# Performance work log

Hardware: AMD Instinct MI355X
Metric: run time of the kernel (lower is better)

Reference implementation:

```python
import jax, jax.numpy as jnp
import numpy as np


def setup_inputs() -> dict:
    key = jax.random.key(0)
    k1, k2 = jax.random.split(key)
    B, H, W, D = 2, 160, 192, 160
    X = jax.random.normal(k1, (B, H, W, D, 2), dtype=jnp.float32)
    deformation = jax.random.normal(k2, (B, H, W, D, 3), dtype=jnp.float32)
    return {"X": X, "deformation": deformation}


def reference(X, deformation):
    # X: (B,H,W,D,2); warp the first channel by the dense deformation field.
    B, H, W, D, _ = X.shape
    Y = X[..., 0:1]                     # (B,H,W,D,1) volume to warp
    N = H * W * D

    # Identity grid, matching tf.meshgrid(x,y,z) 'xy' semantics: shape (H,W,D),
    # x varies along axis1 (width), y along axis0 (height), z along axis2 (depth).
    ys, xs, zs = jnp.meshgrid(
        jnp.arange(H, dtype=jnp.float32),
        jnp.arange(W, dtype=jnp.float32),
        jnp.arange(D, dtype=jnp.float32),
        indexing='ij')

    d = deformation.reshape(B, N, 3)
    x = xs.reshape(-1)[None, :] + d[..., 0]   # (B,N)
    y = ys.reshape(-1)[None, :] + d[..., 1]
    z = zs.reshape(-1)[None, :] + d[..., 2]

    x0 = jnp.floor(x).astype(jnp.int32); x1 = x0 + 1
    y0 = jnp.floor(y).astype(jnp.int32); y1 = y0 + 1
    z0 = jnp.floor(z).astype(jnp.int32); z1 = z0 + 1

    x0 = jnp.clip(x0, 0, W - 1); x1 = jnp.clip(x1, 0, W - 1)
    y0 = jnp.clip(y0, 0, H - 1); y1 = jnp.clip(y1, 0, H - 1)
    z0 = jnp.clip(z0, 0, D - 1); z1 = jnp.clip(z1, 0, D - 1)

    flat = Y.reshape(B, N, 1)           # (B, H*W*D, C=1)

    def gather(yy, xx, zz):
        idx = (yy * (W * D) + xx * D + zz)[..., None]   # (B,N,1)
        return jnp.take_along_axis(flat, idx, axis=1)

    p000 = gather(y0, x0, z0); p001 = gather(y0, x0, z1)
    p010 = gather(y0, x1, z0); p011 = gather(y0, x1, z1)
    p100 = gather(y1, x0, z0); p101 = gather(y1, x0, z1)
    p110 = gather(y1, x1, z0); p111 = gather(y1, x1, z1)

    # Weights use the CLIPPED corner coordinates (faithful to the original).
    x0f = x0.astype(jnp.float32); x1f = x1.astype(jnp.float32)
    y0f = y0.astype(jnp.float32); y1f = y1.astype(jnp.float32)
    z0f = z0.astype(jnp.float32); z1f = z1.astype(jnp.float32)

    w000 = ((y1f - y) * (x1f - x) * (z1f - z))[..., None]
    w001 = ((y1f - y) * (x1f - x) * (z - z0f))[..., None]
    w010 = ((y1f - y) * (x - x0f) * (z1f - z))[..., None]
    w011 = ((y1f - y) * (x - x0f) * (z - z0f))[..., None]
    w100 = ((y - y0f) * (x1f - x) * (z1f - z))[..., None]
    w101 = ((y - y0f) * (x1f - x) * (z - z0f))[..., None]
    w110 = ((y - y0f) * (x - x0f) * (z1f - z))[..., None]
    w111 = ((y - y0f) * (x - x0f) * (z - z0f))[..., None]

    out = (w000 * p000 + w001 * p001 + w010 * p010 + w011 * p011 +
           w100 * p100 + w101 * p101 + w110 * p110 + w111 * p111)
    return out.reshape(B, H, W, D, 1)
```

## Files before the change

kernel.cpp:

```cpp
#include <hip/hip_runtime.h>

#define BB 2
#define HH 160
#define WW 192
#define DD 160
#define NN (HH * WW * DD)
#define TOTAL (BB * NN)

__device__ inline unsigned short f2bf(float f) {
    unsigned u = __builtin_bit_cast(unsigned, f);
    u += 0x7FFFu + ((u >> 16) & 1u);
    return (unsigned short)(u >> 16);
}
__device__ inline float bf2f_lo(unsigned v) {
    return __builtin_bit_cast(float, v << 16);
}
__device__ inline float bf2f_hi(unsigned v) {
    return __builtin_bit_cast(float, v & 0xFFFF0000u);
}

struct __attribute__((packed, aligned(2))) u32u { unsigned v; };
struct __attribute__((packed, aligned(8))) f6u  { float a, b, c, d, e, f; };

__global__ __launch_bounds__(256)
void compact_ch0_bf16_kernel(const float4* __restrict__ X4,
                             ushort4* __restrict__ C4) {
    const int i = blockIdx.x * 256 + threadIdx.x;
    const float4 a = X4[4 * i];
    const float4 b = X4[4 * i + 1];
    const float4 c = X4[4 * i + 2];
    const float4 d = X4[4 * i + 3];
    ushort4 lo, hi;
    lo.x = f2bf(a.x); lo.y = f2bf(a.z); lo.z = f2bf(b.x); lo.w = f2bf(b.z);
    hi.x = f2bf(c.x); hi.y = f2bf(c.z); hi.z = f2bf(d.x); hi.w = f2bf(d.z);
    C4[2 * i]     = lo;
    C4[2 * i + 1] = hi;
}

__global__ __launch_bounds__(256)
void SpatialDeformer3D_kernel(const unsigned short* __restrict__ C,
                              const float* __restrict__ def,
                              float* __restrict__ out) {
    const int t  = blockIdx.x * 256 + threadIdx.x;
    const int n0 = t * 2;

    const int b    = n0 / NN;
    const int rem  = n0 - b * NN;
    const int h    = rem / (WW * DD);
    const int rem2 = rem - h * (WW * DD);
    const int w    = rem2 / DD;
    const int d0   = rem2 - w * DD;

    const f6u dv = *(const f6u*)(def + (size_t)n0 * 3);
    const float dxs[2] = {dv.a, dv.d};
    const float dys[2] = {dv.b, dv.e};
    const float dzs[2] = {dv.c, dv.f};

    const unsigned short* Cb = C + (size_t)b * NN;
    float res[2];

#pragma unroll
    for (int k = 0; k < 2; ++k) {
        const float x = (float)w + dxs[k];
        const float y = (float)h + dys[k];
        const float z = (float)(d0 + k) + dzs[k];

        int ix0 = (int)floorf(x);
        int iy0 = (int)floorf(y);
        int iz0 = (int)floorf(z);
        int ix1 = ix0 + 1, iy1 = iy0 + 1;
        ix0 = min(max(ix0, 0), WW - 1); ix1 = min(max(ix1, 0), WW - 1);
        iy0 = min(max(iy0, 0), HH - 1); iy1 = min(max(iy1, 0), HH - 1);
        const int czlo = min(max(iz0, 0), DD - 1);
        const int czhi = min(max(iz0 + 1, 0), DD - 1);
        const int zb   = min(max(iz0, 0), DD - 2);

        const float wx0 = (float)ix1 - x, wx1 = x - (float)ix0;
        const float wy0 = (float)iy1 - y, wy1 = y - (float)iy0;
        const float wz0 = (float)czhi - z, wz1 = z - (float)czlo;

        const bool lo_is_v0 = (czlo == zb);
        const bool hi_is_v1 = (czhi == zb + 1);

        const int r00 = iy0 * (WW * DD) + ix0 * DD + zb;
        const int r01 = iy0 * (WW * DD) + ix1 * DD + zb;
        const int r10 = iy1 * (WW * DD) + ix0 * DD + zb;
        const int r11 = iy1 * (WW * DD) + ix1 * DD + zb;

        const unsigned g00 = ((const u32u*)(Cb + r00))->v;
        const unsigned g01 = ((const u32u*)(Cb + r01))->v;
        const unsigned g10 = ((const u32u*)(Cb + r10))->v;
        const unsigned g11 = ((const u32u*)(Cb + r11))->v;

        const float v00l = bf2f_lo(g00), v00h = bf2f_hi(g00);
        const float v01l = bf2f_lo(g01), v01h = bf2f_hi(g01);
        const float v10l = bf2f_lo(g10), v10h = bf2f_hi(g10);
        const float v11l = bf2f_lo(g11), v11h = bf2f_hi(g11);

        const float p000 = lo_is_v0 ? v00l : v00h;
        const float p001 = hi_is_v1 ? v00h : v00l;
        const float p010 = lo_is_v0 ? v01l : v01h;
        const float p011 = hi_is_v1 ? v01h : v01l;
        const float p100 = lo_is_v0 ? v10l : v10h;
        const float p101 = hi_is_v1 ? v10h : v10l;
        const float p110 = lo_is_v0 ? v11l : v11h;
        const float p111 = hi_is_v1 ? v11h : v11l;

        res[k] =
            wy0 * (wx0 * (wz0 * p000 + wz1 * p001) + wx1 * (wz0 * p010 + wz1 * p011)) +
            wy1 * (wx0 * (wz0 * p100 + wz1 * p101) + wx1 * (wz0 * p110 + wz1 * p111));
    }

    *(float2*)(out + n0) = make_float2(res[0], res[1]);
}

__global__ __launch_bounds__(256)
void SpatialDeformer3D_direct_kernel(const float* __restrict__ X,
                                     const float* __restrict__ def,
                                     float* __restrict__ out) {
    const int n = blockIdx.x * 256 + threadIdx.x;
    const int b    = n / NN;
    const int rem  = n - b * NN;
    const int h    = rem / (WW * DD);
    const int rem2 = rem - h * (WW * DD);
    const int w    = rem2 / DD;
    const int d    = rem2 - w * DD;

    const float* dp = def + (size_t)n * 3;
    const float x = (float)w + dp[0];
    const float y = (float)h + dp[1];
    const float z = (float)d + dp[2];

    int ix0 = (int)floorf(x);
    int iy0 = (int)floorf(y);
    int iz0 = (int)floorf(z);
    int ix1 = ix0 + 1, iy1 = iy0 + 1, iz1 = iz0 + 1;
    ix0 = min(max(ix0, 0), WW - 1); ix1 = min(max(ix1, 0), WW - 1);
    iy0 = min(max(iy0, 0), HH - 1); iy1 = min(max(iy1, 0), HH - 1);
    iz0 = min(max(iz0, 0), DD - 1); iz1 = min(max(iz1, 0), DD - 1);

    const float wx0 = (float)ix1 - x, wx1 = x - (float)ix0;
    const float wy0 = (float)iy1 - y, wy1 = y - (float)iy0;
    const float wz0 = (float)iz1 - z, wz1 = z - (float)iz0;

    const float* Xb = X + (size_t)b * (2u * (size_t)NN);
    const int ry0 = iy0 * (WW * DD), ry1 = iy1 * (WW * DD);
    const int rx0 = ix0 * DD,        rx1 = ix1 * DD;

    const float p000 = Xb[(size_t)(ry0 + rx0 + iz0) * 2];
    const float p001 = Xb[(size_t)(ry0 + rx0 + iz1) * 2];
    const float p010 = Xb[(size_t)(ry0 + rx1 + iz0) * 2];
    const float p011 = Xb[(size_t)(ry0 + rx1 + iz1) * 2];
    const float p100 = Xb[(size_t)(ry1 + rx0 + iz0) * 2];
    const float p101 = Xb[(size_t)(ry1 + rx0 + iz1) * 2];
    const float p110 = Xb[(size_t)(ry1 + rx1 + iz0) * 2];
    const float p111 = Xb[(size_t)(ry1 + rx1 + iz1) * 2];

    const float r =
        wy0 * (wx0 * (wz0 * p000 + wz1 * p001) + wx1 * (wz0 * p010 + wz1 * p011)) +
        wy1 * (wx0 * (wz0 * p100 + wz1 * p101) + wx1 * (wz0 * p110 + wz1 * p111));

    out[n] = r;
}

extern "C" void kernel_launch(void* const* d_in, const int* in_sizes, int n_in,
                              void* d_out, int out_size, void* d_ws, size_t ws_size,
                              hipStream_t stream) {
    const float* X   = (const float*)d_in[0];
    const float* def = (const float*)d_in[1];
    float* out = (float*)d_out;

    const size_t need = (size_t)TOTAL * sizeof(unsigned short);
    if (ws_size >= need) {
        unsigned short* C = (unsigned short*)d_ws;
        compact_ch0_bf16_kernel<<<(TOTAL / 8) / 256, 256, 0, stream>>>(
            (const float4*)X, (ushort4*)C);
        SpatialDeformer3D_kernel<<<(TOTAL / 2) / 256, 256, 0, stream>>>(C, def, out);
    } else {
        SpatialDeformer3D_direct_kernel<<<TOTAL / 256, 256, 0, stream>>>(X, def, out);
    }
}
```

Before: 258.8 us.

## Stage bf16 neighborhood tile in LDS for trilinear gather

Replaces the per-thread global gather kernel with a block-tiled kernel. Each block cooperatively copies a 10x17 row neighborhood (full depth, bf16) around its 8 output columns into shared memory, then serves the corner reads from LDS. Samples whose floor coordinates fall outside the ±4 halo fall back to global loads. This trades random L2/HBM gathers for a large redundant tile load per block, about 54KB of LDS, which limits occupancy and multiplies the total data read.

```diff
diff --git a/kernel.cpp b/kernel.cpp
--- a/kernel.cpp
+++ b/kernel.cpp
@@ -7,10 +7,20 @@
 #define NN (HH * WW * DD)
 #define TOTAL (BB * NN)
 
+#define TW   8
+#define TNX  17
+#define TNY  10
+#define NROWS (TNY * TNX)
+#define CHUNKS (NROWS * 20)
+#define NTHREADS 640
+
 __device__ inline unsigned short f2bf(float f) {
     unsigned u = __builtin_bit_cast(unsigned, f);
     u += 0x7FFFu + ((u >> 16) & 1u);
     return (unsigned short)(u >> 16);
+}
+__device__ inline float bf2f(unsigned short v) {
+    return __builtin_bit_cast(float, (unsigned)v << 16);
 }
 __device__ inline float bf2f_lo(unsigned v) {
     return __builtin_bit_cast(float, v << 16);
@@ -37,40 +47,58 @@
     C4[2 * i + 1] = hi;
 }
 
-__global__ __launch_bounds__(256)
-void SpatialDeformer3D_kernel(const unsigned short* __restrict__ C,
-                              const float* __restrict__ def,
-                              float* __restrict__ out) {
-    const int t  = blockIdx.x * 256 + threadIdx.x;
-    const int n0 = t * 2;
-
-    const int b    = n0 / NN;
-    const int rem  = n0 - b * NN;
-    const int h    = rem / (WW * DD);
-    const int rem2 = rem - h * (WW * DD);
-    const int w    = rem2 / DD;
-    const int d0   = rem2 - w * DD;
+__global__ __launch_bounds__(NTHREADS, 4)
+void SpatialDeformer3D_lds_kernel(const unsigned short* __restrict__ C,
+                                  const float* __restrict__ def,
+                                  float* __restrict__ out) {
+    __shared__ __align__(16) unsigned short tile[NROWS * DD];
+
+    const int bid = blockIdx.x;
+    const int b   = bid / (HH * (WW / TW));
+    const int r0  = bid - b * (HH * (WW / TW));
+    const int h   = r0 / (WW / TW);
+    const int W0  = (r0 - h * (WW / TW)) * TW;
+
+    const unsigned short* Cb = C + (size_t)b * NN;
+    const int tid = threadIdx.x;
+
+    for (int c = tid; c < CHUNKS; c += NTHREADS) {
+        const int row = c / 20;
+        const int sub = c - row * 20;
+        const int qy  = row / TNX;
+        const int qx  = row - qy * TNX;
+        const int iy  = min(max(h - 4 + qy, 0), HH - 1);
+        const int ix  = min(max(W0 - 4 + qx, 0), WW - 1);
+        const ulonglong2 v =
+            *(const ulonglong2*)(Cb + (size_t)(iy * (WW * DD) + ix * DD) + sub * 8);
+        *(ulonglong2*)(tile + (size_t)c * 8) = v;
+    }
+    __syncthreads();
+
+    const int wl = tid / 80;
+    const int dp = tid - wl * 80;
+    const int w  = W0 + wl;
+    const int d0 = dp * 2;
+    const int n0 = b * NN + h * (WW * DD) + w * DD + d0;
 
     const f6u dv = *(const f6u*)(def + (size_t)n0 * 3);
     const float dxs[2] = {dv.a, dv.d};
     const float dys[2] = {dv.b, dv.e};
     const float dzs[2] = {dv.c, dv.f};
 
-    const unsigned short* Cb = C + (size_t)b * NN;
     float res[2];
-
 #pragma unroll
     for (int k = 0; k < 2; ++k) {
         const float x = (float)w + dxs[k];
         const float y = (float)h + dys[k];
         const float z = (float)(d0 + k) + dzs[k];
 
-        int ix0 = (int)floorf(x);
-        int iy0 = (int)floorf(y);
-        int iz0 = (int)floorf(z);
-        int ix1 = ix0 + 1, iy1 = iy0 + 1;
-        ix0 = min(max(ix0, 0), WW - 1); ix1 = min(max(ix1, 0), WW - 1);
-        iy0 = min(max(iy0, 0), HH - 1); iy1 = min(max(iy1, 0), HH - 1);
+        const int fx0 = (int)floorf(x);
+        const int fy0 = (int)floorf(y);
+        const int iz0 = (int)floorf(z);
+
+        const int ix0 = min(max(fx0, 0), WW - 1), ix1 = min(max(fx0 + 1, 0), WW - 1);
+        const int iy0 = min(max(fy0, 0), HH - 1), iy1 = min(max(fy0 + 1, 0), HH - 1);
         const int czlo = min(max(iz0, 0), DD - 1);
         const int czhi = min(max(iz0 + 1, 0), DD - 1);
         const int zb   = min(max(iz0, 0), DD - 2);
@@ -78,33 +106,47 @@
         const float wx0 = (float)ix1 - x, wx1 = x - (float)ix0;
         const float wy0 = (float)iy1 - y, wy1 = y - (float)iy0;
         const float wz0 = (float)czhi - z, wz1 = z - (float)czlo;
-
-        const bool lo_is_v0 = (czlo == zb);
-        const bool hi_is_v1 = (czhi == zb + 1);
-
-        const int r00 = iy0 * (WW * DD) + ix0 * DD + zb;
-        const int r01 = iy0 * (WW * DD) + ix1 * DD + zb;
-        const int r10 = iy1 * (WW * DD) + ix0 * DD + zb;
-        const int r11 = iy1 * (WW * DD) + ix1 * DD + zb;
-
-        const unsigned g00 = ((const u32u*)(Cb + r00))->v;
-        const unsigned g01 = ((const u32u*)(Cb + r01))->v;
-        const unsigned g10 = ((const u32u*)(Cb + r10))->v;
-        const unsigned g11 = ((const u32u*)(Cb + r11))->v;
-
-        const float v00l = bf2f_lo(g00), v00h = bf2f_hi(g00);
-        const float v01l = bf2f_lo(g01), v01h = bf2f_hi(g01);
-        const float v10l = bf2f_lo(g10), v10h = bf2f_hi(g10);
-        const float v11l = bf2f_lo(g11), v11h = bf2f_hi(g11);
-
-        const float p000 = lo_is_v0 ? v00l : v00h;
-        const float p001 = hi_is_v1 ? v00h : v00l;
-        const float p010 = lo_is_v0 ? v01l : v01h;
-        const float p011 = hi_is_v1 ? v01h : v01l;
-        const float p100 = lo_is_v0 ? v10l : v10h;
-        const float p101 = hi_is_v1 ? v10h : v10l;
-        const float p110 = lo_is_v0 ? v11l : v11h;
-        const float p111 = hi_is_v1 ? v11h : v11l;
+        const bool lov = (czlo == zb);
+        const bool hiv = (czhi == zb + 1);
+
+        float p000, p001, p010, p011, p100, p101, p110, p111;
+
+        const bool ok = (fy0 >= h - 4) & (fy0 <= h + 4) &
+                        (fx0 >= W0 - 4) & (fx0 <= W0 + TW + 3);
+        if (ok) {
+            const int ry = (fy0 - (h - 4)) * TNX + (fx0 - (W0 - 4));
+            const int a00 = ry * DD + zb;
+            const int a01 = a00 + DD;
+            const int a10 = a00 + TNX * DD;
+            const int a11 = a10 + DD;
+
+            const float v00l = bf2f(tile[a00]), v00h = bf2f(tile[a00 + 1]);
+            const float v01l = bf2f(tile[a01]), v01h = bf2f(tile[a01 + 1]);
+            const float v10l = bf2f(tile[a10]), v10h = bf2f(tile[a10 + 1]);
+            const float v11l = bf2f(tile[a11]), v11h = bf2f(tile[a11 + 1]);
+
+            p000 = lov ? v00l : v00h;  p001 = hiv ? v00h : v00l;
+            p010 = lov ? v01l : v01h;  p011 = hiv ? v01h : v01l;
+            p100 = lov ? v10l : v10h;  p101 = hiv ? v10h : v10l;
+            p110 = lov ? v11l : v11h;  p111 = hiv ? v11h : v11l;
+        } else {
+            const int r00 = iy0 * (WW * DD) + ix0 * DD + zb;
+            const int r01 = iy0 * (WW * DD) + ix1 * DD + zb;
+            const int r10 = iy1 * (WW * DD) + ix0 * DD + zb;
+            const int r11 = iy1 * (WW * DD) + ix1 * DD + zb;
+            const unsigned g00 = ((const u32u*)(Cb + r00))->v;
+            const unsigned g01 = ((const u32u*)(Cb + r01))->v;
+            const unsigned g10 = ((const u32u*)(Cb + r10))->v;
+            const unsigned g11 = ((const u32u*)(Cb + r11))->v;
+            const float v00l = bf2f_lo(g00), v00h = bf2f_hi(g00);
+            const float v01l = bf2f_lo(g01), v01h = bf2f_hi(g01);
+            const float v10l = bf2f_lo(g10), v10h = bf2f_hi(g10);
+            const float v11l = bf2f_lo(g11), v11h = bf2f_hi(g11);
+            p000 = lov ? v00l : v00h;  p001 = hiv ? v00h : v00l;
+            p010 = lov ? v01l : v01h;  p011 = hiv ? v01h : v01l;
+            p100 = lov ? v10l : v10h;  p101 = hiv ? v10h : v10l;
+            p110 = lov ? v11l : v11h;  p111 = hiv ? v11h : v11l;
+        }
 
         res[k] =
             wy0 * (wx0 * (wz0 * p000 + wz1 * p001) + wx1 * (wz0 * p010 + wz1 * p011)) +
@@ -175,7 +217,8 @@
         unsigned short* C = (unsigned short*)d_ws;
         compact_ch0_bf16_kernel<<<(TOTAL / 8) / 256, 256, 0, stream>>>(
             (const float4*)X, (ushort4*)C);
-        SpatialDeformer3D_kernel<<<(TOTAL / 2) / 256, 256, 0, stream>>>(C, def, out);
+        SpatialDeformer3D_lds_kernel<<<BB * HH * (WW / TW), NTHREADS, 0, stream>>>(
+            C, def, out);
     } else {
         SpatialDeformer3D_direct_kernel<<<TOTAL / 256, 256, 0, stream>>>(X, def, out);
     }
```

Result: slower. 294.4 us (+13.7%).
